# Kernel tuning notes

Measured on AMD Instinct MI355X. Metric: run time of the kernel, lower is better.

## Reference

```python
import jax, jax.numpy as jnp
import numpy as np

B, S, C = 4096, 6, 2048  # batch, num_strips, in_channel
D = C // 8               # query/key projection dim

def setup_inputs() -> dict:
    key = jax.random.key(0)
    k1, k2, k3, k4 = jax.random.split(key, 4)
    sc = 1.0 / np.sqrt(C)
    return {
        "x": jax.random.normal(k1, (B, S, C), dtype=jnp.float32),
        "Wq": jax.random.normal(k2, (D, C), dtype=jnp.float32) * sc,
        "Wk": jax.random.normal(k3, (D, C), dtype=jnp.float32) * sc,
        "Wv": jax.random.normal(k4, (C, C), dtype=jnp.float32) * sc,
        "gamma": jnp.ones((1,), dtype=jnp.float32),
    }

def reference(x, Wq, Wk, Wv, gamma):
    # x: [B, S, C] stacked squeezed strips (feat in the torch code)
    q = jnp.einsum('bsc,dc->bsd', x, Wq)          # [B, S, D]
    k = jnp.einsum('bsc,dc->bsd', x, Wk)          # [B, S, D]
    energy = jnp.einsum('bsd,btd->bst', q, k)     # [B, S, S]
    attention = jax.nn.softmax(energy, axis=-1)   # softmax over keys
    v = jnp.einsum('bsc,dc->bsd', x, Wv)          # [B, S, C]
    out = jnp.einsum('bst,btc->bsc', attention, v)  # [B, S, C]
    out = gamma * out + x                         # gamma-scaled residual
    return out, attention
```

## Files before the change

kernel.cpp:

```cpp
#include <hip/hip_runtime.h>

typedef __attribute__((ext_vector_type(4))) float f32x4;
typedef __attribute__((ext_vector_type(8))) _Float16 f16x8;
typedef __attribute__((ext_vector_type(4))) unsigned short u16x4;
typedef __attribute__((ext_vector_type(8))) unsigned short u16x8;

#define NB 4096
#define NS 6
#define NC 2048
#define MTOT (NB * NS)

static __device__ __forceinline__ unsigned short f2h_bits(float f) {
  _Float16 h = (_Float16)f;
  unsigned short b;
  __builtin_memcpy(&b, &h, 2);
  return b;
}
static __device__ __forceinline__ float h2f(unsigned short b) {
  _Float16 h;
  __builtin_memcpy(&h, &b, 2);
  return (float)h;
}

#define NX4 12582912
#define NW4 262144
#define NV4 1048576
__global__ void prep_all(const float* __restrict__ x, const float* __restrict__ Wq,
                         const float* __restrict__ Wk, const float* __restrict__ Wv,
                         unsigned short* __restrict__ xh, unsigned short* __restrict__ wqk,
                         unsigned short* __restrict__ wvh) {
  long i = blockIdx.x * blockDim.x + threadIdx.x;
  const long stride = (long)gridDim.x * blockDim.x;
  for (; i < NX4 + NW4 + NV4; i += stride) {
    f32x4 v;
    unsigned short* dst;
    long di;
    if (i < NX4) {
      v = reinterpret_cast<const f32x4*>(x)[i];
      dst = xh; di = i;
    } else if (i < NX4 + NW4) {
      const long j = i - NX4;
      const int row = (int)(j >> 9);
      const int col4 = (int)(j & 511);
      const float* src = (row < 256) ? (Wq + (size_t)row * NC)
                                     : (Wk + (size_t)(row - 256) * NC);
      v = reinterpret_cast<const f32x4*>(src)[col4];
      dst = wqk; di = j;
    } else {
      const long j = i - NX4 - NW4;
      v = reinterpret_cast<const f32x4*>(Wv)[j];
      dst = wvh; di = j;
    }
    u16x4 o;
#pragma unroll
    for (int j = 0; j < 4; ++j) o[j] = f2h_bits(v[j]);
    reinterpret_cast<u16x4*>(dst)[di] = o;
  }
}


#define FENCE() asm volatile("" ::: "memory")
#define BAR() do { FENCE(); __builtin_amdgcn_s_barrier(); FENCE(); } while (0)
#define VM4BAR() do { FENCE(); asm volatile("s_waitcnt vmcnt(4)" ::: "memory"); \
                      __builtin_amdgcn_s_barrier(); FENCE(); } while (0)

__device__ __forceinline__ void stage_op(const unsigned short* g, int row0, int k0,
                                         char* ldsOp, int wid, int lane) {
  const int sl = lane ^ ((lane >> 4) & 1) ^ (((lane >> 5) & 1) << 1);
#pragma unroll
  for (int h = 0; h < 2; ++h)
#pragma unroll
    for (int i = 0; i < 2; ++i) {
      const int c = wid * 2 + i;
      const unsigned short* src =
          g + (size_t)(row0 + h * 128 + (c >> 1) * 16 + (sl >> 2)) * 2048 +
          (unsigned)(k0 + (c & 1) * 32 + (sl & 3) * 8);
      __builtin_amdgcn_global_load_lds(
          (__attribute__((address_space(1))) void*)src,
          (__attribute__((address_space(3))) void*)(ldsOp + h * 16384 + c * 1024),
          16, 0, 0);
    }
}

template <int N, bool EPI, bool NFAST>
__global__ void __launch_bounds__(512, 2)
gemm256(const unsigned short* __restrict__ A, const unsigned short* __restrict__ B,
        float* __restrict__ C, const float* __restrict__ resid,
        const float* __restrict__ gam) {
  constexpr int NT = 2048 / 64;
  constexpr int MT = MTOT / 256;
  constexpr int NXT = N / 256;
  constexpr int NWG = MT * NXT;
  constexpr int CPX = NWG / 8;
  __shared__ char lds[131072];

  const int bid = blockIdx.x;
  const int wg = (bid & 7) * CPX + (bid >> 3);
  const int bx = NFAST ? (wg % NXT) : (wg / MT);
  const int by = NFAST ? (wg / NXT) : (wg % MT);
  const int m0 = by * 256, n0 = bx * 256;

  const int t = threadIdx.x;
  const int lane = t & 63;
  const int wid = t >> 6;
  const int wr = wid >> 2, wc = wid & 3;
  const int laneOff = (lane & 15) * 64 + (lane >> 4) * 16;
  const int swzOff = laneOff ^ (((laneOff >> 9) & 1) << 5) ^ (((laneOff >> 8) & 1) << 4);
  const int aBase = wr * 16384 + swzOff;
  const int bBase = 32768 + (wc >> 1) * 16384 + (wc & 1) * 8192 + swzOff;

  f32x4 acc[8][4] = {};

#define WRAPT(TT) ((TT) >= NT ? (TT) - NT : (TT))
#define STAGE_A(TT) stage_op(A, m0, WRAPT(TT) * 64, lds + ((TT) & 1) * 65536, wid, lane)
#define STAGE_B(TT) stage_op(B, n0, WRAPT(TT) * 64, lds + ((TT) & 1) * 65536 + 32768, wid, lane)

  STAGE_A(0);
  STAGE_B(0);
  STAGE_B(1);
  VM4BAR();

  for (int tau = 0; tau < NT; ++tau) {
    char* bufc = lds + (tau & 1) * 65536;
    STAGE_A(tau + 1);
    f16x8 Af[8], Bf[4];
#pragma unroll
    for (int m = 0; m < 4; ++m) {
      Af[m]     = *reinterpret_cast<const f16x8*>(bufc + aBase + (m * 2) * 1024);
      Af[4 + m] = *reinterpret_cast<const f16x8*>(bufc + aBase + 8192 + (m * 2) * 1024);
    }
#pragma unroll
    for (int n = 0; n < 4; ++n)
      Bf[n] = *reinterpret_cast<const f16x8*>(bufc + bBase + (n * 2) * 1024);
    __builtin_amdgcn_s_setprio(1);
#pragma unroll
    for (int m = 0; m < 8; ++m)
#pragma unroll
      for (int n = 0; n < 4; ++n)
        acc[m][n] = __builtin_amdgcn_mfma_f32_16x16x32_f16(Af[m], Bf[n], acc[m][n], 0, 0, 0);
    __builtin_amdgcn_s_setprio(0);
    f16x8 Ag[8], Bg[4];
#pragma unroll
    for (int m = 0; m < 4; ++m) {
      Ag[m]     = *reinterpret_cast<const f16x8*>(bufc + aBase + (m * 2 + 1) * 1024);
      Ag[4 + m] = *reinterpret_cast<const f16x8*>(bufc + aBase + 8192 + (m * 2 + 1) * 1024);
    }
#pragma unroll
    for (int n = 0; n < 4; ++n)
      Bg[n] = *reinterpret_cast<const f16x8*>(bufc + bBase + (n * 2 + 1) * 1024);
    BAR();
    STAGE_B(tau + 2);
    VM4BAR();
    __builtin_amdgcn_s_setprio(1);
#pragma unroll
    for (int m = 0; m < 8; ++m)
#pragma unroll
      for (int n = 0; n < 4; ++n)
        acc[m][n] = __builtin_amdgcn_mfma_f32_16x16x32_f16(Ag[m], Bg[n], acc[m][n], 0, 0, 0);
    __builtin_amdgcn_s_setprio(0);
    BAR();
  }

#undef STAGE_A
#undef STAGE_B
#undef WRAPT

  const float g = EPI ? gam[0] : 0.f;
#pragma unroll
  for (int m = 0; m < 8; ++m)
#pragma unroll
    for (int n = 0; n < 4; ++n)
#pragma unroll
      for (int j = 0; j < 4; ++j) {
        const int r = m0 + wr * 128 + m * 16 + (lane >> 4) * 4 + j;
        const int c = n0 + wc * 64 + n * 16 + (lane & 15);
        const size_t idx = (size_t)r * (size_t)N + (size_t)c;
        float v = acc[m][n][j];
        if (EPI) v = g * v + resid[idx];
        C[idx] = v;
      }
}

__global__ void __launch_bounds__(256)
attn_fuse(const float* __restrict__ QK,
          const unsigned short* __restrict__ xh,
          float* __restrict__ attn_out,
          unsigned short* __restrict__ y)
{
  __shared__ float qk[NS * 512];
  __shared__ float eng[36];
  __shared__ float att[36];
  const int b = blockIdx.x;
  const int t = threadIdx.x;
  {
    const f32x4* src = reinterpret_cast<const f32x4*>(QK + (size_t)b * (NS * 512));
    f32x4* dst = reinterpret_cast<f32x4*>(qk);
    for (int i = t; i < (NS * 512) / 4; i += 256) dst[i] = src[i];
  }
  __syncthreads();
  if (t < 144) {
    const int s = t / 24;
    const int rem = t - s * 24;
    const int u = rem >> 2;
    const int sub = rem & 3;
    const float* qr = qk + s * 512;
    const float* kr = qk + u * 512 + 256;
    float sum = 0.f;
    const int d0 = sub * 64;
#pragma unroll 4
    for (int d = 0; d < 64; ++d) sum += qr[d0 + d] * kr[d0 + d];
    sum += __shfl_xor(sum, 1);
    sum += __shfl_xor(sum, 2);
    if (sub == 0) eng[s * 6 + u] = sum;
  }
  __syncthreads();
  if (t < 6) {
    float e[6];
#pragma unroll
    for (int u = 0; u < 6; ++u) e[u] = eng[t * 6 + u];
    float mx = e[0];
#pragma unroll
    for (int u = 1; u < 6; ++u) mx = fmaxf(mx, e[u]);
    float p[6];
    float sm = 0.f;
#pragma unroll
    for (int u = 0; u < 6; ++u) { p[u] = expf(e[u] - mx); sm += p[u]; }
    const float inv = 1.0f / sm;
#pragma unroll
    for (int u = 0; u < 6; ++u) {
      const float a = p[u] * inv;
      att[t * 6 + u] = a;
      attn_out[(size_t)b * 36 + t * 6 + u] = a;
    }
  }
  __syncthreads();
  const unsigned short* xb = xh + (size_t)b * (NS * NC);
  unsigned short* yb = y + (size_t)b * (NS * NC);
  const int c0 = t * 8;
  f32x4 xv[12];
#pragma unroll
  for (int u = 0; u < 6; ++u) {
    u16x8 v = *reinterpret_cast<const u16x8*>(xb + u * NC + c0);
#pragma unroll
    for (int j = 0; j < 4; ++j) {
      xv[2 * u][j] = h2f(v[j]);
      xv[2 * u + 1][j] = h2f(v[4 + j]);
    }
  }
#pragma unroll
  for (int s = 0; s < 6; ++s) {
    f32x4 a0 = 0.f, a1 = 0.f;
#pragma unroll
    for (int u = 0; u < 6; ++u) {
      const float w = att[s * 6 + u];
      a0 += w * xv[2 * u];
      a1 += w * xv[2 * u + 1];
    }
    u16x8 o;
#pragma unroll
    for (int j = 0; j < 4; ++j) { o[j] = f2h_bits(a0[j]); o[4 + j] = f2h_bits(a1[j]); }
    *reinterpret_cast<u16x8*>(yb + s * NC + c0) = o;
  }
}

extern "C" void kernel_launch(void* const* d_in, const int* in_sizes, int n_in,
                              void* d_out, int out_size, void* d_ws, size_t ws_size,
                              hipStream_t stream) {
  (void)in_sizes; (void)n_in; (void)out_size; (void)ws_size;
  const float* x   = (const float*)d_in[0];
  const float* Wq  = (const float*)d_in[1];
  const float* Wk  = (const float*)d_in[2];
  const float* Wv  = (const float*)d_in[3];
  const float* gam = (const float*)d_in[4];
  float* out = (float*)d_out;
  float* attn_out = out + (size_t)MTOT * NC;

  char* ws = (char*)d_ws;
  unsigned short* xh  = (unsigned short*)(ws);
  unsigned short* yb  = (unsigned short*)(ws + 100663296ull);
  unsigned short* wqk = (unsigned short*)(ws + 201326592ull);
  unsigned short* wvh = (unsigned short*)(ws + 203423744ull);
  float*          qkb = (float*)(ws + 211812352ull);

  prep_all<<<2048, 256, 0, stream>>>(x, Wq, Wk, Wv, xh, wqk, wvh);

  gemm256<512, false, false><<<192, 512, 0, stream>>>(
      xh, wqk, qkb, nullptr, nullptr);

  attn_fuse<<<NB, 256, 0, stream>>>(qkb, xh, attn_out, yb);

  gemm256<2048, true, true><<<768, 512, 0, stream>>>(
      yb, wvh, out, x, gam);
}
```

Baseline: 407.9 us.

## Switch GEMM to 32x32x16 MFMA with new LDS layout and software-pipelined fragment loads

Replaces the 16x16x32 f16 MFMA tiling with 32x32x16 MFMA instructions, re-laying out the LDS staging so each 1KB chunk holds 32 rows by 16 k-elements with a new XOR swizzle. The k-loop is split into four quarter-steps, with LDS fragment loads for the next quarter interleaved with MFMAs on the current one. The aim is fewer MFMA issues and LDS reads per tile and better overlap of LDS latency with compute. The s_setprio hints are dropped and the epilogue index mapping changes to match the 32x32 accumulator layout, which risks layout or bank-conflict mistakes.

```diff
diff --git a/kernel.cpp b/kernel.cpp
--- a/kernel.cpp
+++ b/kernel.cpp
@@ -1,6 +1,7 @@
 #include <hip/hip_runtime.h>
 
 typedef __attribute__((ext_vector_type(4))) float f32x4;
+typedef __attribute__((ext_vector_type(16))) float f32x16;
 typedef __attribute__((ext_vector_type(8))) _Float16 f16x8;
 typedef __attribute__((ext_vector_type(4))) unsigned short u16x4;
 typedef __attribute__((ext_vector_type(8))) unsigned short u16x8;
@@ -66,20 +67,18 @@
 
 __device__ __forceinline__ void stage_op(const unsigned short* g, int row0, int k0,
                                          char* ldsOp, int wid, int lane) {
-  const int sl = lane ^ ((lane >> 4) & 1) ^ (((lane >> 5) & 1) << 1);
-#pragma unroll
-  for (int h = 0; h < 2; ++h)
-#pragma unroll
-    for (int i = 0; i < 2; ++i) {
-      const int c = wid * 2 + i;
-      const unsigned short* src =
-          g + (size_t)(row0 + h * 128 + (c >> 1) * 16 + (sl >> 2)) * 2048 +
-          (unsigned)(k0 + (c & 1) * 32 + (sl & 3) * 8);
-      __builtin_amdgcn_global_load_lds(
-          (__attribute__((address_space(1))) void*)src,
-          (__attribute__((address_space(3))) void*)(ldsOp + h * 16384 + c * 1024),
-          16, 0, 0);
-    }
+  const int rr = lane >> 1;
+  const int kh = (lane & 1) ^ ((lane >> 3) & 1);
+#pragma unroll
+  for (int i = 0; i < 4; ++i) {
+    const int c = wid * 4 + i;
+    const unsigned short* src =
+        g + (size_t)(row0 + (c >> 2) * 32 + rr) * 2048 +
+        (unsigned)(k0 + (c & 3) * 16 + kh * 8);
+    __builtin_amdgcn_global_load_lds(
+        (__attribute__((address_space(1))) void*)src,
+        (__attribute__((address_space(3))) void*)(ldsOp + c * 1024), 16, 0, 0);
+  }
 }
 
 template <int N, bool EPI, bool NFAST>
@@ -104,16 +103,32 @@
   const int lane = t & 63;
   const int wid = t >> 6;
   const int wr = wid >> 2, wc = wid & 3;
-  const int laneOff = (lane & 15) * 64 + (lane >> 4) * 16;
-  const int swzOff = laneOff ^ (((laneOff >> 9) & 1) << 5) ^ (((laneOff >> 8) & 1) << 4);
-  const int aBase = wr * 16384 + swzOff;
-  const int bBase = 32768 + (wc >> 1) * 16384 + (wc & 1) * 8192 + swzOff;
-
-  f32x4 acc[8][4] = {};
+  const int laneOff = (lane & 31) * 32 + (lane >> 5) * 16;
+  const int swz = laneOff ^ (((laneOff >> 7) & 1) << 4);
+
+  f32x16 acc[4][2] = {};
+  f16x8 A0_[4], A1_[4], B0_[2], B1_[2];
 
 #define WRAPT(TT) ((TT) >= NT ? (TT) - NT : (TT))
 #define STAGE_A(TT) stage_op(A, m0, WRAPT(TT) * 64, lds + ((TT) & 1) * 65536, wid, lane)
 #define STAGE_B(TT) stage_op(B, n0, WRAPT(TT) * 64, lds + ((TT) & 1) * 65536 + 32768, wid, lane)
+
+#define LDQ(AV, BV, q) do { \
+    AV[0] = *reinterpret_cast<const f16x8*>(bufc + ((wr * 4 + 0) * 4 + (q)) * 1024 + swz); \
+    AV[1] = *reinterpret_cast<const f16x8*>(bufc + ((wr * 4 + 1) * 4 + (q)) * 1024 + swz); \
+    AV[2] = *reinterpret_cast<const f16x8*>(bufc + ((wr * 4 + 2) * 4 + (q)) * 1024 + swz); \
+    AV[3] = *reinterpret_cast<const f16x8*>(bufc + ((wr * 4 + 3) * 4 + (q)) * 1024 + swz); \
+    BV[0] = *reinterpret_cast<const f16x8*>(bufc + 32768 + ((wc * 2 + 0) * 4 + (q)) * 1024 + swz); \
+    BV[1] = *reinterpret_cast<const f16x8*>(bufc + 32768 + ((wc * 2 + 1) * 4 + (q)) * 1024 + swz); \
+  } while (0)
+
+#define MFQ(AV, BV) do { \
+    _Pragma("unroll") \
+    for (int mt = 0; mt < 4; ++mt) \
+      _Pragma("unroll") \
+      for (int nt = 0; nt < 2; ++nt) \
+        acc[mt][nt] = __builtin_amdgcn_mfma_f32_32x32x16_f16(AV[mt], BV[nt], acc[mt][nt], 0, 0, 0); \
+  } while (0)
 
   STAGE_A(0);
   STAGE_B(0);
@@ -123,59 +138,37 @@
   for (int tau = 0; tau < NT; ++tau) {
     char* bufc = lds + (tau & 1) * 65536;
     STAGE_A(tau + 1);
-    f16x8 Af[8], Bf[4];
-#pragma unroll
-    for (int m = 0; m < 4; ++m) {
-      Af[m]     = *reinterpret_cast<const f16x8*>(bufc + aBase + (m * 2) * 1024);
-      Af[4 + m] = *reinterpret_cast<const f16x8*>(bufc + aBase + 8192 + (m * 2) * 1024);
-    }
-#pragma unroll
-    for (int n = 0; n < 4; ++n)
-      Bf[n] = *reinterpret_cast<const f16x8*>(bufc + bBase + (n * 2) * 1024);
-    __builtin_amdgcn_s_setprio(1);
-#pragma unroll
-    for (int m = 0; m < 8; ++m)
-#pragma unroll
-      for (int n = 0; n < 4; ++n)
-        acc[m][n] = __builtin_amdgcn_mfma_f32_16x16x32_f16(Af[m], Bf[n], acc[m][n], 0, 0, 0);
-    __builtin_amdgcn_s_setprio(0);
-    f16x8 Ag[8], Bg[4];
-#pragma unroll
-    for (int m = 0; m < 4; ++m) {
-      Ag[m]     = *reinterpret_cast<const f16x8*>(bufc + aBase + (m * 2 + 1) * 1024);
-      Ag[4 + m] = *reinterpret_cast<const f16x8*>(bufc + aBase + 8192 + (m * 2 + 1) * 1024);
-    }
-#pragma unroll
-    for (int n = 0; n < 4; ++n)
-      Bg[n] = *reinterpret_cast<const f16x8*>(bufc + bBase + (n * 2 + 1) * 1024);
+    LDQ(A0_, B0_, 0);
+    LDQ(A1_, B1_, 1);
+    MFQ(A0_, B0_);
+    LDQ(A0_, B0_, 2);
+    MFQ(A1_, B1_);
+    LDQ(A1_, B1_, 3);
+    MFQ(A0_, B0_);
     BAR();
     STAGE_B(tau + 2);
     VM4BAR();
-    __builtin_amdgcn_s_setprio(1);
-#pragma unroll
-    for (int m = 0; m < 8; ++m)
-#pragma unroll
-      for (int n = 0; n < 4; ++n)
-        acc[m][n] = __builtin_amdgcn_mfma_f32_16x16x32_f16(Ag[m], Bg[n], acc[m][n], 0, 0, 0);
-    __builtin_amdgcn_s_setprio(0);
+    MFQ(A1_, B1_);
     BAR();
   }
 
+#undef MFQ
+#undef LDQ
 #undef STAGE_A
 #undef STAGE_B
 #undef WRAPT
 
   const float g = EPI ? gam[0] : 0.f;
 #pragma unroll
-  for (int m = 0; m < 8; ++m)
-#pragma unroll
-    for (int n = 0; n < 4; ++n)
-#pragma unroll
-      for (int j = 0; j < 4; ++j) {
-        const int r = m0 + wr * 128 + m * 16 + (lane >> 4) * 4 + j;
-        const int c = n0 + wc * 64 + n * 16 + (lane & 15);
+  for (int mt = 0; mt < 4; ++mt)
+#pragma unroll
+    for (int nt = 0; nt < 2; ++nt)
+#pragma unroll
+      for (int i = 0; i < 16; ++i) {
+        const int r = m0 + wr * 128 + mt * 32 + (i & 3) + 8 * (i >> 2) + 4 * (lane >> 5);
+        const int c = n0 + wc * 64 + nt * 32 + (lane & 31);
         const size_t idx = (size_t)r * (size_t)N + (size_t)c;
-        float v = acc[m][n][j];
+        float v = acc[mt][nt][i];
         if (EPI) v = g * v + resid[idx];
         C[idx] = v;
       }
```

Result: slower. 553.9 us (+35.8%).
